# Performance work log

Measured on AMD Instinct MI355X. Metric: run time of the kernel, lower is better.

## Reference

```python
import jax, jax.numpy as jnp
import numpy as np

B, S, R, V, C, K, H = 256, 64, 256, 2000, 10, 6, 4
D = 256
DH = D // H
NEG = -1e9


def setup_inputs() -> dict:
    key = jax.random.key(0)
    ks = jax.random.split(key, 32)
    w = lambda i, shape: jax.random.normal(ks[i], shape, jnp.float32) * 0.05
    inp = {}
    inp["vis_emb"] = jax.random.normal(ks[0], (B * S, D), jnp.float32)
    # multi-hot concept vectors (sparse 0/1)
    inp["basic"] = (jax.random.uniform(ks[1], (R, V)) < 0.01).astype(jnp.float32)
    inp["crucial"] = (jax.random.uniform(ks[2], (R, V)) < 0.01).astype(jnp.float32)
    # to_b / to_k linears
    inp["Wtb"], inp["btb"] = w(3, (V, D)), w(4, (D,))
    inp["Wtk"], inp["btk"] = w(5, (V, D)), w(6, (D,))
    # cross attention (rule2vis): q/k/v/out projections
    inp["Wq"], inp["bq"] = w(7, (D, D)), w(8, (D,))
    inp["Wk"], inp["bk"] = w(9, (D, D)), w(10, (D,))
    inp["Wv"], inp["bv"] = w(11, (D, D)), w(12, (D,))
    inp["Wo"], inp["bo"] = w(13, (D, D)), w(14, (D,))
    # per-class GAT stacks: GAT(256->128), GAT(128->64), Linear(64->K)
    inp["W1"], inp["a1s"], inp["a1d"], inp["b1"] = w(15, (C, D, 128)), w(16, (C, 128)), w(17, (C, 128)), w(18, (C, 128))
    inp["W2"], inp["a2s"], inp["a2d"], inp["b2"] = w(19, (C, 128, 64)), w(20, (C, 64)), w(21, (C, 64)), w(22, (C, 64))
    inp["Wl"], inp["bl"] = w(23, (C, 64, K)), w(24, (C, K))
    # rule-graph adjacency: symmetric + self loops (PyG GATConv adds self loops)
    a0 = jax.random.uniform(ks[25], (R, R)) < 0.05
    inp["adj"] = a0 | a0.T | jnp.eye(R, dtype=bool)
    # class membership mask: each rule node belongs to one class head
    cls = jax.random.randint(ks[26], (R,), 0, C)
    inp["mask"] = (cls[None, :] == jnp.arange(C)[:, None]).astype(jnp.int32)
    return inp


def _gat(h, W, a_s, a_d, b, adj_bias):
    # h: [B,R,Fin] -> [B,R,Fout]; single-head PyG-style GATConv over dense adj
    hW = h @ W                                             # [B,R,F]
    e_dst = jnp.einsum('brf,f->br', hW, a_d)               # dst term
    e_src = jnp.einsum('brf,f->br', hW, a_s)               # src term
    e = jax.nn.leaky_relu(e_dst[:, :, None] + e_src[:, None, :], 0.2)  # [B,Rdst,Rsrc]
    alpha = jax.nn.softmax(e + adj_bias[None], axis=-1)
    return jnp.einsum('bij,bjf->bif', alpha, hW) + b


def reference(vis_emb, basic, crucial, Wtb, btb, Wtk, btk, Wq, bq, Wk, bk, Wv, bv,
              Wo, bo, W1, a1s, a1d, b1, W2, a2s, a2d, b2, Wl, bl, adj, mask):
    # rule embeddings: to_b(basic) + to_k(crucial)
    rule = basic @ Wtb + btb + crucial @ Wtk + btk         # [R,D]
    kv = vis_emb.reshape(B, S, D)
    q = jnp.broadcast_to(rule[None], (B, R, D))
    Q = (q @ Wq + bq).reshape(B, R, H, DH)
    Kx = (kv @ Wk + bk).reshape(B, S, H, DH)
    Vx = (kv @ Wv + bv).reshape(B, S, H, DH)
    att = jnp.einsum('brhd,bshd->bhrs', Q, Kx) / jnp.sqrt(jnp.float32(DH))
    att = jax.nn.softmax(att, axis=-1)
    emb = jnp.einsum('bhrs,bshd->brhd', att, Vx).reshape(B, R, D) @ Wo + bo  # [B,R,D]

    adj_bias = jnp.where(adj, 0.0, NEG).astype(emb.dtype)  # [R,R]
    outs = []
    for c in range(C):  # small fixed number of class heads
        h = emb * mask[c].astype(emb.dtype)[None, :, None]
        h = jax.nn.relu(_gat(h, W1[c], a1s[c], a1d[c], b1[c], adj_bias))
        h = _gat(h, W2[c], a2s[c], a2d[c], b2[c], adj_bias)  # dropout = eval identity
        h = h @ Wl[c] + bl[c]                                # [B,R,K]
        outs.append(jax.nn.log_softmax(h.sum(axis=1), axis=1))
    return jnp.stack(outs)  # [C,B,K]
```

## Files before the change

kernel.cpp:

```cpp
#include <hip/hip_runtime.h>
#include <stdint.h>

#define NB 256
#define NS 64
#define NR 256
#define NV 2000
#define NC 10
#define NK 6
#define ND 256

typedef __attribute__((ext_vector_type(8))) short bf16x8;
typedef __attribute__((ext_vector_type(4))) float f32x4;

__device__ __forceinline__ float bf2f(uint16_t u) {
  return __uint_as_float(((uint32_t)u) << 16);
}
__device__ __forceinline__ uint16_t f2bf(float f) {
  uint32_t x = __float_as_uint(f);
  x += 0x7FFFu + ((x >> 16) & 1u);
  return (uint16_t)(x >> 16);
}

__global__ __launch_bounds__(256) void k_front(
    const void* __restrict__ adj_raw, const int* __restrict__ mask,
    const float* __restrict__ W2, const float* __restrict__ a2s,
    const float* __restrict__ a2d,
    uint32_t* __restrict__ adjbits, int* __restrict__ cls,
    int* __restrict__ lists, int* __restrict__ cnt,
    int* __restrict__ deg, uint8_t* __restrict__ nbr,
    int8_t* __restrict__ midx,
    float* __restrict__ ud2, float* __restrict__ us2,
    const float* __restrict__ Wo, const float* __restrict__ Wk,
    const float* __restrict__ Wv, const float* __restrict__ W1,
    uint16_t* __restrict__ WOT, uint16_t* __restrict__ WKVT,
    uint16_t* __restrict__ W1T,
    const float* __restrict__ basic, const float* __restrict__ cruc,
    const float* __restrict__ Wtb, const float* __restrict__ btb,
    const float* __restrict__ Wtk, const float* __restrict__ btk,
    const float* __restrict__ Wq, const float* __restrict__ bq,
    uint16_t* __restrict__ Qbf,
    const float* __restrict__ vis, const float* __restrict__ bk,
    const float* __restrict__ bv,
    uint16_t* __restrict__ KX, uint16_t* __restrict__ VX)
{
  __shared__ char smem[33792];
  int bid = blockIdx.x;
  int tid = threadIdx.x;
  if (bid < 11) {
    if (bid == 0) {
      int* s_is4 = (int*)smem;
      if (tid == 0) *s_is4 = 1;
      __syncthreads();
      const uint32_t* u = (const uint32_t*)adj_raw;
      int ok = 1;
      for (int idx = tid; idx < 16384; idx += 256) {
        uint32_t v = u[idx];
        if (!(v == 0u || v == 1u || v == 0x3F800000u)) ok = 0;
      }
      if (!ok) atomicAnd(s_is4, 0);
      __syncthreads();
      int is4 = *s_is4;
      const uint8_t* b8 = (const uint8_t*)adj_raw;
      int dg = 0;
      for (int w = 0; w < 8; ++w) {
        uint32_t word = 0;
        for (int jb = 0; jb < 32; ++jb) {
          int j = w * 32 + jb;
          int bit = is4 ? (u[tid * 256 + j] != 0u) : (b8[tid * 256 + j] != 0);
          if (bit) {
            word |= (1u << jb);
            if (dg < 64) nbr[tid * 64 + dg] = (uint8_t)j;
            dg++;
          }
        }
        adjbits[tid * 8 + w] = word;
      }
      deg[tid] = (dg > 64) ? 64 : dg;
      int c = 0;
      for (int cc = 0; cc < NC; ++cc) if (mask[cc * 256 + tid] != 0) c = cc;
      cls[tid] = c;
      __syncthreads();
      if (tid == 0) {
        int cn[NC];
        for (int i = 0; i < NC; ++i) cn[i] = 0;
        for (int r = 0; r < 256; ++r) {
          int cc = cls[r];
          if (cn[cc] < 64) lists[cc * 64 + cn[cc]] = r;
          cn[cc]++;
        }
        for (int i = 0; i < NC; ++i) cnt[i] = (cn[i] > 64) ? 64 : cn[i];
        for (int i = 0; i < NC * 256; ++i) midx[i] = -1;
        for (int cc = 0; cc < NC; ++cc)
          for (int i = 0; i < cnt[cc]; ++i)
            midx[cc * 256 + lists[cc * 64 + i]] = (int8_t)i;
      }
    } else {
      int c = bid - 1;
      if (tid < 128) {
        float s1 = 0.f, s2 = 0.f;
        for (int g = 0; g < 64; ++g) {
          float w = W2[(c * 128 + tid) * 64 + g];
          s1 += w * a2d[c * 64 + g];
          s2 += w * a2s[c * 64 + g];
        }
        ud2[c * 128 + tid] = s1;
        us2[c * 128 + tid] = s2;
      }
    }
  } else if (bid < 139) {
    float (*ts)[65] = (float(*)[65])smem;
    int pb = bid - 11;
    const float* src;
    uint16_t* dst;
    int ncols, kt, nt;
    if (pb < 16)      { src = Wo; dst = WOT; ncols = 256; kt = pb >> 2; nt = pb & 3; }
    else if (pb < 32) { int t = pb - 16; src = Wk; dst = WKVT; ncols = 256; kt = t >> 2; nt = t & 3; }
    else if (pb < 48) { int t = pb - 32; src = Wv; dst = WKVT + 256 * 256; ncols = 256; kt = t >> 2; nt = t & 3; }
    else { int t = pb - 48; int c = t >> 3; int tt = t & 7;
           src = W1 + (long)c * 256 * 128; dst = W1T + (long)c * 128 * 256;
           ncols = 128; kt = tt >> 1; nt = tt & 1; }
    for (int idx = tid; idx < 4096; idx += 256) {
      int i = idx >> 6, j = idx & 63;
      ts[i][j] = src[(long)(kt * 64 + i) * ncols + nt * 64 + j];
    }
    __syncthreads();
    for (int idx = tid; idx < 4096; idx += 256) {
      int i = idx >> 6, j = idx & 63;
      dst[(long)(nt * 64 + i) * 256 + kt * 64 + j] = f2bf(ts[j][i]);
    }
  } else if (bid < 395) {
    float* row_s  = (float*)smem;
    float* rule_s = row_s + 2048;
    int*   nzi    = (int*)(rule_s + 256);
    float* nzv    = (float*)(nzi + 128);
    int*   nzcp   = (int*)(nzv + 128);
    int r = bid - 139;
    float acc = btb[tid] + btk[tid];
    for (int m = 0; m < 2; ++m) {
      const float* src = m ? cruc : basic;
      const float* W   = m ? Wtk : Wtb;
      for (int idx = tid; idx < 2048; idx += 256)
        row_s[idx] = (idx < NV) ? src[r * NV + idx] : 0.0f;
      if (tid == 0) *nzcp = 0;
      __syncthreads();
      if (tid < 64) {
        int base = 0;
        for (int ch = 0; ch < 32; ++ch) {
          int idx = ch * 64 + tid;
          float v = row_s[idx];
          unsigned long long bm = __ballot(v != 0.0f);
          if (v != 0.0f) {
            int pos = base + (int)__popcll(bm & ((1ull << tid) - 1ull));
            if (pos < 128) { nzi[pos] = idx; nzv[pos] = v; }
          }
          base += (int)__popcll(bm);
        }
        if (tid == 0) *nzcp = (base > 128) ? 128 : base;
      }
      __syncthreads();
      int n = *nzcp;
      for (int t = 0; t < n; ++t) acc += nzv[t] * W[nzi[t] * 256 + tid];
      __syncthreads();
    }
    rule_s[tid] = acc;
    __syncthreads();
    float q = bq[tid];
    for (int k2 = 0; k2 < 256; ++k2) q += rule_s[k2] * Wq[k2 * 256 + tid];
    Qbf[r * 256 + tid] = f2bf(q * 0.125f);
  } else {
    uint16_t* A_s = (uint16_t*)smem;
    int t = bid - 395;
    int bx = t & 255, by = t >> 8;
    int lane = tid & 63, w = tid >> 6;
    int r15 = lane & 15, kg = lane >> 4;
    long m0 = (long)bx * 64;
    int n0 = by * 64 + w * 16;
    for (int idx = tid; idx < 2048; idx += 256) {
      int r = idx >> 5, ch = idx & 31;
      const float4* p = (const float4*)&vis[(m0 + r) * 256 + ch * 8];
      float4 v0 = p[0], v1 = p[1];
      uint4 wd;
      wd.x = (uint32_t)f2bf(v0.x) | ((uint32_t)f2bf(v0.y) << 16);
      wd.y = (uint32_t)f2bf(v0.z) | ((uint32_t)f2bf(v0.w) << 16);
      wd.z = (uint32_t)f2bf(v1.x) | ((uint32_t)f2bf(v1.y) << 16);
      wd.w = (uint32_t)f2bf(v1.z) | ((uint32_t)f2bf(v1.w) << 16);
      *(uint4*)&A_s[r * 264 + ch * 8] = wd;
    }
    __syncthreads();
    const uint16_t* bptr = &WKVT[(long)(n0 + r15) * 256 + kg * 8];
    f32x4 acc[4];
    #pragma unroll
    for (int mt = 0; mt < 4; ++mt) acc[mt] = (f32x4){0.f, 0.f, 0.f, 0.f};
    #pragma unroll
    for (int ks = 0; ks < 8; ++ks) {
      bf16x8 bfr = *(const bf16x8*)(bptr + ks * 32);
      #pragma unroll
      for (int mt = 0; mt < 4; ++mt) {
        bf16x8 afr = *(const bf16x8*)&A_s[(mt * 16 + r15) * 264 + kg * 8 + ks * 32];
        acc[mt] = __builtin_amdgcn_mfma_f32_16x16x32_bf16(afr, bfr, acc[mt], 0, 0, 0);
      }
    }
    int col = n0 + r15;
    float bb = (col < 256) ? bk[col] : bv[col - 256];
    uint16_t* outp = (col < 256) ? KX : VX;
    int oc = (col < 256) ? col : col - 256;
    #pragma unroll
    for (int mt = 0; mt < 4; ++mt)
      #pragma unroll
      for (int j = 0; j < 4; ++j) {
        long row = m0 + mt * 16 + kg * 4 + j;
        outp[row * 256 + oc] = f2bf(acc[mt][j] + bb);
      }
  }
}

__global__ __launch_bounds__(512) void k_attn(const uint16_t* __restrict__ Qbf,
                         const uint16_t* __restrict__ KX, const uint16_t* __restrict__ VX,
                         uint16_t* __restrict__ EMB)
{
  __shared__ uint16_t p_s[128 * 72];
  __shared__ uint16_t vt_s[64 * 72];
  int tid = threadIdx.x;
  int lane = tid & 63, w = tid >> 6;
  int r15 = lane & 15, kg = lane >> 4;
  int b = blockIdx.x >> 1;
  int rbase = (blockIdx.x & 1) * 128;
  for (int h = 0; h < 4; ++h) {
    __syncthreads();
    for (int idx = tid; idx < 2048; idx += 512) {
      int s = idx >> 5, d2 = (idx & 31) * 2;
      uint32_t v = *(const uint32_t*)&VX[((long)(b * 64 + s)) * 256 + h * 64 + d2];
      vt_s[d2 * 72 + s] = (uint16_t)(v & 0xffff);
      vt_s[(d2 + 1) * 72 + s] = (uint16_t)(v >> 16);
    }
    __syncthreads();
    f32x4 sacc[4];
    #pragma unroll
    for (int nt = 0; nt < 4; ++nt) sacc[nt] = (f32x4){0.f, 0.f, 0.f, 0.f};
    #pragma unroll
    for (int ks = 0; ks < 2; ++ks) {
      bf16x8 afr = *(const bf16x8*)&Qbf[(long)(rbase + w * 16 + r15) * 256 + h * 64 + ks * 32 + kg * 8];
      #pragma unroll
      for (int nt = 0; nt < 4; ++nt) {
        bf16x8 bfr = *(const bf16x8*)&KX[((long)(b * 64 + nt * 16 + r15)) * 256 + h * 64 + ks * 32 + kg * 8];
        sacc[nt] = __builtin_amdgcn_mfma_f32_16x16x32_bf16(afr, bfr, sacc[nt], 0, 0, 0);
      }
    }
    #pragma unroll
    for (int j = 0; j < 4; ++j) {
      float m = sacc[0][j];
      #pragma unroll
      for (int nt = 1; nt < 4; ++nt) m = fmaxf(m, sacc[nt][j]);
      m = fmaxf(m, __shfl_xor(m, 1));
      m = fmaxf(m, __shfl_xor(m, 2));
      m = fmaxf(m, __shfl_xor(m, 4));
      m = fmaxf(m, __shfl_xor(m, 8));
      float pv[4];
      float sum = 0.f;
      #pragma unroll
      for (int nt = 0; nt < 4; ++nt) { pv[nt] = __expf(sacc[nt][j] - m); sum += pv[nt]; }
      sum += __shfl_xor(sum, 1);
      sum += __shfl_xor(sum, 2);
      sum += __shfl_xor(sum, 4);
      sum += __shfl_xor(sum, 8);
      float rs = 1.0f / sum;
      #pragma unroll
      for (int nt = 0; nt < 4; ++nt)
        p_s[(w * 16 + kg * 4 + j) * 72 + nt * 16 + r15] = f2bf(pv[nt] * rs);
    }
    f32x4 oacc[4];
    #pragma unroll
    for (int nt = 0; nt < 4; ++nt) oacc[nt] = (f32x4){0.f, 0.f, 0.f, 0.f};
    #pragma unroll
    for (int ks = 0; ks < 2; ++ks) {
      bf16x8 afr = *(const bf16x8*)&p_s[(w * 16 + r15) * 72 + ks * 32 + kg * 8];
      #pragma unroll
      for (int nt = 0; nt < 4; ++nt) {
        bf16x8 bfr = *(const bf16x8*)&vt_s[(nt * 16 + r15) * 72 + ks * 32 + kg * 8];
        oacc[nt] = __builtin_amdgcn_mfma_f32_16x16x32_bf16(afr, bfr, oacc[nt], 0, 0, 0);
      }
    }
    #pragma unroll
    for (int nt = 0; nt < 4; ++nt)
      #pragma unroll
      for (int j = 0; j < 4; ++j) {
        long row = (long)(b * 256 + rbase + w * 16 + kg * 4 + j);
        EMB[row * 256 + h * 64 + nt * 16 + r15] = f2bf(oacc[nt][j]);
      }
  }
}

__global__ __launch_bounds__(256) void k_wo(uint16_t* __restrict__ EMB,
                    const uint16_t* __restrict__ WOT, const float* __restrict__ bo)
{
  __shared__ uint16_t A_s[64 * 264];
  int tid = threadIdx.x;
  int lane = tid & 63, w = tid >> 6;
  int r15 = lane & 15, kg = lane >> 4;
  long m0 = (long)blockIdx.x * 64;
  for (int idx = tid; idx < 2048; idx += 256) {
    int r = idx >> 5, ch = idx & 31;
    uint4 v = *(const uint4*)&EMB[(m0 + r) * 256 + ch * 8];
    *(uint4*)&A_s[r * 264 + ch * 8] = v;
  }
  __syncthreads();
  #pragma unroll
  for (int nt = 0; nt < 4; ++nt) {
    int n0 = nt * 64 + w * 16;
    const uint16_t* bptr = &WOT[(long)(n0 + r15) * 256 + kg * 8];
    f32x4 acc[4];
    #pragma unroll
    for (int mt = 0; mt < 4; ++mt) acc[mt] = (f32x4){0.f, 0.f, 0.f, 0.f};
    #pragma unroll
    for (int ks = 0; ks < 8; ++ks) {
      bf16x8 bfr = *(const bf16x8*)(bptr + ks * 32);
      #pragma unroll
      for (int mt = 0; mt < 4; ++mt) {
        bf16x8 afr = *(const bf16x8*)&A_s[(mt * 16 + r15) * 264 + kg * 8 + ks * 32];
        acc[mt] = __builtin_amdgcn_mfma_f32_16x16x32_bf16(afr, bfr, acc[mt], 0, 0, 0);
      }
    }
    int col = n0 + r15;
    float bb = bo[col];
    #pragma unroll
    for (int mt = 0; mt < 4; ++mt)
      #pragma unroll
      for (int j = 0; j < 4; ++j) {
        long row = m0 + mt * 16 + kg * 4 + j;
        EMB[row * 256 + col] = f2bf(acc[mt][j] + bb);
      }
  }
}

__global__ __launch_bounds__(1024) void k_gat(
    const uint16_t* __restrict__ EMB, const uint16_t* __restrict__ W1T,
    const float* __restrict__ a1d, const float* __restrict__ a1s,
    const int* __restrict__ lists, const int* __restrict__ cnt_g,
    const int* __restrict__ deg_g, const uint8_t* __restrict__ nbr_g,
    const int8_t* __restrict__ midx_g,
    const float* __restrict__ b1, const float* __restrict__ ud2_g,
    const float* __restrict__ us2_g, const float* __restrict__ W2,
    const float* __restrict__ b2, const float* __restrict__ Wl,
    const float* __restrict__ bl, float* __restrict__ out)
{
  __shared__ uint16_t alpha_s[256 * 72];
  __shared__ uint16_t hwt_s[128 * 72];
  __shared__ float e1d_s[256], e1s_s[256], rd1_s[256];
  __shared__ float e2d_s[256], e2s_s[256], rd2_s[256];
  __shared__ float a1d_s[128], a1s_s[128], b1_s[128], ud2_s[128], us2_s[128];
  __shared__ float t_s[128];
  __shared__ int   list_s[64];
  float (*tpart)[128] = (float(*)[128])alpha_s;
  float* wj_s = rd1_s;
  float* svec = (float*)hwt_s;
  float* lvec = (float*)(hwt_s + 256);
  int tid = threadIdx.x;
  int lane = tid & 63, w = tid >> 6;
  int r15 = lane & 15, kg = lane >> 4;
  int c = blockIdx.x >> 8, b = blockIdx.x & 255;
  int n = cnt_g[c];
  if (tid < 64) list_s[tid] = (tid < n) ? lists[c * 64 + tid] : 0;
  if (tid < 128) {
    a1d_s[tid] = a1d[c * 128 + tid];
    a1s_s[tid] = a1s[c * 128 + tid];
    b1_s[tid]  = b1[c * 128 + tid];
    ud2_s[tid] = ud2_g[c * 128 + tid];
    us2_s[tid] = us2_g[c * 128 + tid];
  }
  if (tid < 256) { e1d_s[tid] = 0.f; e1s_s[tid] = 0.f; }
  int r = tid >> 2, q = tid & 3;
  int dg = deg_g[r];
  int t0 = q * 16;
  int ncnt = dg - t0; ncnt = (ncnt < 0) ? 0 : (ncnt > 16 ? 16 : ncnt);
  const uint32_t* np = (const uint32_t*)&nbr_g[r * 64 + t0];
  uint32_t nbw0 = np[0], nbw1 = np[1], nbw2 = np[2], nbw3 = np[3];
  __syncthreads();
  int mt = w & 3, nh = w >> 2;
  int colA = nh * 32 + r15, colB = colA + 16;
  const uint16_t* bptr = &W1T[((long)c * 128 + colA) * 256 + kg * 8];
  const uint16_t* arow = &EMB[((long)b * 256 + list_s[mt * 16 + r15]) * 256 + kg * 8];
  f32x4 acc0 = (f32x4){0.f, 0.f, 0.f, 0.f};
  f32x4 acc1 = (f32x4){0.f, 0.f, 0.f, 0.f};
  if (mt * 16 < n) {
    #pragma unroll
    for (int ks = 0; ks < 8; ++ks) {
      bf16x8 b0 = *(const bf16x8*)(bptr + ks * 32);
      bf16x8 b1f = *(const bf16x8*)(bptr + 16 * 256 + ks * 32);
      bf16x8 afr = *(const bf16x8*)(arow + ks * 32);
      acc0 = __builtin_amdgcn_mfma_f32_16x16x32_bf16(afr, b0, acc0, 0, 0, 0);
      acc1 = __builtin_amdgcn_mfma_f32_16x16x32_bf16(afr, b1f, acc1, 0, 0, 0);
    }
  }
  {
    uint2 pA, pB;
    pA.x = (uint32_t)f2bf(acc0[0]) | ((uint32_t)f2bf(acc0[1]) << 16);
    pA.y = (uint32_t)f2bf(acc0[2]) | ((uint32_t)f2bf(acc0[3]) << 16);
    pB.x = (uint32_t)f2bf(acc1[0]) | ((uint32_t)f2bf(acc1[1]) << 16);
    pB.y = (uint32_t)f2bf(acc1[2]) | ((uint32_t)f2bf(acc1[3]) << 16);
    *(uint2*)&hwt_s[colA * 72 + mt * 16 + kg * 4] = pA;
    *(uint2*)&hwt_s[colB * 72 + mt * 16 + kg * 4] = pB;
    float adA = a1d_s[colA], adB = a1d_s[colB];
    float asA = a1s_s[colA], asB = a1s_s[colB];
    #pragma unroll
    for (int j = 0; j < 4; ++j) {
      float pd = acc0[j] * adA + acc1[j] * adB;
      float ps = acc0[j] * asA + acc1[j] * asB;
      pd += __shfl_xor(pd, 1); pd += __shfl_xor(pd, 2);
      pd += __shfl_xor(pd, 4); pd += __shfl_xor(pd, 8);
      ps += __shfl_xor(ps, 1); ps += __shfl_xor(ps, 2);
      ps += __shfl_xor(ps, 4); ps += __shfl_xor(ps, 8);
      if (r15 == 0) {
        int jm = mt * 16 + kg * 4 + j;
        e2d_s[nh * 64 + jm] = pd;
        e2s_s[nh * 64 + jm] = ps;
      }
    }
  }
  __syncthreads();
  for (int idx = tid; idx < 4608; idx += 1024)
    *(uint2*)&alpha_s[idx * 4] = (uint2){0u, 0u};
  if (tid < 64 && tid < n) {
    float sd = e2d_s[tid] + e2d_s[tid + 64] + e2d_s[tid + 128] + e2d_s[tid + 192];
    float ss = e2s_s[tid] + e2s_s[tid + 64] + e2s_s[tid + 128] + e2s_s[tid + 192];
    int rr = list_s[tid];
    e1d_s[rr] = sd;
    e1s_s[rr] = ss;
  }
  __syncthreads();
  {
    float e1dv = e1d_s[r];
    float den = 0.f;
    #define NB_CHUNK(WORD, BASE)                                            \
      _Pragma("unroll")                                                     \
      for (int ii = 0; ii < 4; ++ii) {                                      \
        if (BASE + ii < ncnt) {                                             \
          int j = (int)((WORD >> (ii * 8)) & 255u);                         \
          float e = e1dv + e1s_s[j];                                        \
          e = fmaxf(e, 0.2f * e);                                           \
          e = fminf(e, 60.f);                                               \
          float wv = __expf(e);                                             \
          den += wv;                                                        \
          int mi = midx_g[c * 256 + j];                                     \
          if (mi >= 0) alpha_s[r * 72 + mi] = f2bf(wv);                     \
        }                                                                   \
      }
    NB_CHUNK(nbw0, 0) NB_CHUNK(nbw1, 4) NB_CHUNK(nbw2, 8) NB_CHUNK(nbw3, 12)
    #undef NB_CHUNK
    den += __shfl_xor(den, 1);
    den += __shfl_xor(den, 2);
    if (q == 0) rd1_s[r] = 1.0f / den;
  }
  __syncthreads();
  f32x4 g[8];
  #pragma unroll
  for (int nt = 0; nt < 8; ++nt) g[nt] = (f32x4){0.f, 0.f, 0.f, 0.f};
  int kslices = (n > 32) ? 2 : 1;
  for (int ks = 0; ks < kslices; ++ks) {
    bf16x8 afr = *(const bf16x8*)&alpha_s[(w * 16 + r15) * 72 + ks * 32 + kg * 8];
    #pragma unroll
    for (int nt = 0; nt < 8; ++nt) {
      bf16x8 bfr = *(const bf16x8*)&hwt_s[(nt * 16 + r15) * 72 + ks * 32 + kg * 8];
      g[nt] = __builtin_amdgcn_mfma_f32_16x16x32_bf16(afr, bfr, g[nt], 0, 0, 0);
    }
  }
  {
    float rd1v[4];
    #pragma unroll
    for (int j = 0; j < 4; ++j) rd1v[j] = rd1_s[w * 16 + kg * 4 + j];
    float ed[4] = {0.f, 0.f, 0.f, 0.f}, es[4] = {0.f, 0.f, 0.f, 0.f};
    #pragma unroll
    for (int nt = 0; nt < 8; ++nt) {
      float uf = ud2_s[nt * 16 + r15], sf = us2_s[nt * 16 + r15];
      float bf = b1_s[nt * 16 + r15];
      #pragma unroll
      for (int j = 0; j < 4; ++j) {
        float gv = fmaxf(g[nt][j] * rd1v[j] + bf, 0.f);
        g[nt][j] = gv;
        ed[j] += gv * uf;
        es[j] += gv * sf;
      }
    }
    __syncthreads();
    #pragma unroll
    for (int j = 0; j < 4; ++j) {
      ed[j] += __shfl_xor(ed[j], 1); ed[j] += __shfl_xor(ed[j], 2);
      ed[j] += __shfl_xor(ed[j], 4); ed[j] += __shfl_xor(ed[j], 8);
      es[j] += __shfl_xor(es[j], 1); es[j] += __shfl_xor(es[j], 2);
      es[j] += __shfl_xor(es[j], 4); es[j] += __shfl_xor(es[j], 8);
      if (r15 == 0) {
        e2d_s[w * 16 + kg * 4 + j] = ed[j];
        e2s_s[w * 16 + kg * 4 + j] = es[j];
      }
    }
  }
  __syncthreads();
  {
    float e2dv = e2d_s[r];
    float den2 = 0.f;
    #define NB_CHUNK(WORD, BASE)                                            \
      _Pragma("unroll")                                                     \
      for (int ii = 0; ii < 4; ++ii) {                                      \
        if (BASE + ii < ncnt) {                                             \
          int j = (int)((WORD >> (ii * 8)) & 255u);                         \
          float e = e2dv + e2s_s[j];                                        \
          e = fmaxf(e, 0.2f * e);                                           \
          e = fminf(e, 60.f);                                               \
          den2 += __expf(e);                                                \
        }                                                                   \
      }
    NB_CHUNK(nbw0, 0) NB_CHUNK(nbw1, 4) NB_CHUNK(nbw2, 8) NB_CHUNK(nbw3, 12)
    #undef NB_CHUNK
    den2 += __shfl_xor(den2, 1);
    den2 += __shfl_xor(den2, 2);
    if (q == 0) rd2_s[r] = 1.0f / den2;
  }
  __syncthreads();
  {
    float e2sv = e2s_s[r];
    float wj = 0.f;
    #define NB_CHUNK(WORD, BASE)                                            \
      _Pragma("unroll")                                                     \
      for (int ii = 0; ii < 4; ++ii) {                                      \
        if (BASE + ii < ncnt) {                                             \
          int i2 = (int)((WORD >> (ii * 8)) & 255u);                        \
          float e = e2d_s[i2] + e2sv;                                       \
          e = fmaxf(e, 0.2f * e);                                           \
          e = fminf(e, 60.f);                                               \
          wj += __expf(e) * rd2_s[i2];                                      \
        }                                                                   \
      }
    NB_CHUNK(nbw0, 0) NB_CHUNK(nbw1, 4) NB_CHUNK(nbw2, 8) NB_CHUNK(nbw3, 12)
    #undef NB_CHUNK
    wj += __shfl_xor(wj, 1);
    wj += __shfl_xor(wj, 2);
    if (q == 0) wj_s[r] = wj;
  }
  __syncthreads();
  {
    float wjv[4];
    #pragma unroll
    for (int j = 0; j < 4; ++j) wjv[j] = wj_s[w * 16 + kg * 4 + j];
    #pragma unroll
    for (int nt = 0; nt < 8; ++nt) {
      float tp = wjv[0] * g[nt][0] + wjv[1] * g[nt][1] + wjv[2] * g[nt][2] + wjv[3] * g[nt][3];
      tp += __shfl_xor(tp, 16);
      tp += __shfl_xor(tp, 32);
      if (kg == 0) tpart[w][nt * 16 + r15] = tp;
    }
  }
  __syncthreads();
  if (tid < 128) {
    float s = 0.f;
    #pragma unroll
    for (int w2 = 0; w2 < 16; ++w2) s += tpart[w2][tid];
    t_s[tid] = s;
  }
  __syncthreads();
  {
    int col = tid & 63, fg = tid >> 6;
    float sp = 0.f;
    #pragma unroll
    for (int i = 0; i < 8; ++i) {
      int f = fg * 8 + i;
      sp += t_s[f] * W2[((long)c * 128 + f) * 64 + col];
    }
    tpart[fg][col] = sp;
  }
  __syncthreads();
  if (tid < 64) {
    float s = 256.0f * b2[c * 64 + tid];
    #pragma unroll
    for (int fg = 0; fg < 16; ++fg) s += tpart[fg][tid];
    svec[tid] = s;
  }
  __syncthreads();
  if (tid < 6) {
    float lg = 256.0f * bl[c * 6 + tid];
    for (int f = 0; f < 64; ++f) lg += svec[f] * Wl[((long)c * 64 + f) * 6 + tid];
    lvec[tid] = lg;
  }
  __syncthreads();
  if (tid == 0) {
    float mm = lvec[0];
    for (int k2 = 1; k2 < 6; ++k2) mm = fmaxf(mm, lvec[k2]);
    float ss = 0.f;
    for (int k2 = 0; k2 < 6; ++k2) ss += __expf(lvec[k2] - mm);
    float lse = mm + __logf(ss);
    for (int k2 = 0; k2 < 6; ++k2) out[((long)c * 256 + b) * 6 + k2] = lvec[k2] - lse;
  }
}

extern "C" void kernel_launch(void* const* d_in, const int* in_sizes, int n_in,
                              void* d_out, int out_size, void* d_ws, size_t ws_size,
                              hipStream_t stream)
{
  const float* vis   = (const float*)d_in[0];
  const float* basic = (const float*)d_in[1];
  const float* cruc  = (const float*)d_in[2];
  const float* Wtb   = (const float*)d_in[3];
  const float* btb   = (const float*)d_in[4];
  const float* Wtk   = (const float*)d_in[5];
  const float* btk   = (const float*)d_in[6];
  const float* Wq    = (const float*)d_in[7];
  const float* bq    = (const float*)d_in[8];
  const float* Wk    = (const float*)d_in[9];
  const float* bk    = (const float*)d_in[10];
  const float* Wv    = (const float*)d_in[11];
  const float* bv    = (const float*)d_in[12];
  const float* Wo    = (const float*)d_in[13];
  const float* bo    = (const float*)d_in[14];
  const float* W1    = (const float*)d_in[15];
  const float* a1s   = (const float*)d_in[16];
  const float* a1d   = (const float*)d_in[17];
  const float* b1    = (const float*)d_in[18];
  const float* W2    = (const float*)d_in[19];
  const float* a2s   = (const float*)d_in[20];
  const float* a2d   = (const float*)d_in[21];
  const float* b2    = (const float*)d_in[22];
  const float* Wl    = (const float*)d_in[23];
  const float* bl    = (const float*)d_in[24];
  const void*  adj   = d_in[25];
  const int*   mask  = (const int*)d_in[26];
  float* out = (float*)d_out;
  char* ws = (char*)d_ws;

  uint16_t* QBF  = (uint16_t*)(ws + 0);
  uint32_t* ADJ  = (uint32_t*)(ws + 262144);
  int*      CLS  = (int*)(ws + 270336);
  int*      LST  = (int*)(ws + 271360);
  int*      CNT  = (int*)(ws + 273920);
  int*      DEG  = (int*)(ws + 273984);
  uint8_t*  NBR  = (uint8_t*)(ws + 275008);
  int8_t*   MIDX = (int8_t*)(ws + 291392);
  float*    UD2  = (float*)(ws + 293952);
  float*    US2  = (float*)(ws + 299072);
  uint16_t* WOT  = (uint16_t*)(ws + 304192);
  uint16_t* WKVT = (uint16_t*)(ws + 435264);
  uint16_t* W1T  = (uint16_t*)(ws + 697408);
  uint16_t* KX   = (uint16_t*)(ws + 1352768);
  uint16_t* VX   = (uint16_t*)(ws + 9741376);
  uint16_t* EMB  = (uint16_t*)(ws + 18129984);

  hipLaunchKernelGGL(k_front, dim3(2443), dim3(256), 0, stream,
                     adj, mask, W2, a2s, a2d, ADJ, CLS, LST, CNT, DEG, NBR, MIDX,
                     UD2, US2,
                     Wo, Wk, Wv, W1, WOT, WKVT, W1T,
                     basic, cruc, Wtb, btb, Wtk, btk, Wq, bq, QBF,
                     vis, bk, bv, KX, VX);
  hipLaunchKernelGGL(k_attn, dim3(512), dim3(512), 0, stream, QBF, KX, VX, EMB);
  hipLaunchKernelGGL(k_wo, dim3(1024), dim3(256), 0, stream, EMB, WOT, bo);
  hipLaunchKernelGGL(k_gat, dim3(2560), dim3(1024), 0, stream,
                     EMB, W1T, a1d, a1s, LST, CNT, DEG, NBR, MIDX,
                     b1, UD2, US2, W2, b2, Wl, bl, out);
}
```

Measured before the change: 416.8 us.

## Process two batch elements per GAT block to amortize per-class setup

Each k_gat block now handles a pair of batch elements (A and B) for one class, halving the grid to 1280 blocks. Class constants, W1T fragments and neighbor lists are loaded once and reused for both, interleaving twice the MFMA and exp work between barriers for more ILP. midx is staged in shared memory instead of read from global. This doubles LDS use and register pressure (two sets of g accumulators), which may reduce occupancy to one block per CU.

```diff
diff --git a/kernel.cpp b/kernel.cpp
--- a/kernel.cpp
+++ b/kernel.cpp
@@ -343,23 +343,35 @@
     const float* __restrict__ b2, const float* __restrict__ Wl,
     const float* __restrict__ bl, float* __restrict__ out)
 {
-  __shared__ uint16_t alpha_s[256 * 72];
-  __shared__ uint16_t hwt_s[128 * 72];
-  __shared__ float e1d_s[256], e1s_s[256], rd1_s[256];
-  __shared__ float e2d_s[256], e2s_s[256], rd2_s[256];
+  __shared__ uint16_t alphaA[256 * 72], alphaB[256 * 72];
+  __shared__ uint16_t hwtA[128 * 72], hwtB[128 * 72];
+  __shared__ float e1dA_s[256], e1sA_s[256], e1dB_s[256], e1sB_s[256];
+  __shared__ float rd1A_s[256], rd1B_s[256];
+  __shared__ float e2dA_s[256], e2sA_s[256], e2dB_s[256], e2sB_s[256];
+  __shared__ float rd2A_s[256], rd2B_s[256];
   __shared__ float a1d_s[128], a1s_s[128], b1_s[128], ud2_s[128], us2_s[128];
-  __shared__ float t_s[128];
+  __shared__ float t_sA[128], t_sB[128];
   __shared__ int   list_s[64];
-  float (*tpart)[128] = (float(*)[128])alpha_s;
-  float* wj_s = rd1_s;
-  float* svec = (float*)hwt_s;
-  float* lvec = (float*)(hwt_s + 256);
+  __shared__ int8_t midx_s[256];
+  float (*tpartA)[128] = (float(*)[128])alphaA;
+  float (*tpartB)[128] = (float(*)[128])alphaB;
+  float* wjA_s = rd1A_s;
+  float* wjB_s = rd1B_s;
+  float* svecA = (float*)hwtA;
+  float* lvecA = (float*)(hwtA + 256);
+  float* svecB = (float*)hwtB;
+  float* lvecB = (float*)(hwtB + 256);
   int tid = threadIdx.x;
   int lane = tid & 63, w = tid >> 6;
   int r15 = lane & 15, kg = lane >> 4;
-  int c = blockIdx.x >> 8, b = blockIdx.x & 255;
+  int c = blockIdx.x >> 7, bp = blockIdx.x & 127;
+  int bA = bp * 2, bB = bp * 2 + 1;
   int n = cnt_g[c];
   if (tid < 64) list_s[tid] = (tid < n) ? lists[c * 64 + tid] : 0;
+  if (tid >= 64 && tid < 128) {
+    int i = tid - 64;
+    ((uint32_t*)midx_s)[i] = ((const uint32_t*)(midx_g + (long)c * 256))[i];
+  }
   if (tid < 128) {
     a1d_s[tid] = a1d[c * 128 + tid];
     a1s_s[tid] = a1s[c * 128 + tid];
@@ -367,7 +379,10 @@
     ud2_s[tid] = ud2_g[c * 128 + tid];
     us2_s[tid] = us2_g[c * 128 + tid];
   }
-  if (tid < 256) { e1d_s[tid] = 0.f; e1s_s[tid] = 0.f; }
+  if (tid < 256) {
+    e1dA_s[tid] = 0.f; e1sA_s[tid] = 0.f;
+    e1dB_s[tid] = 0.f; e1sB_s[tid] = 0.f;
+  }
   int r = tid >> 2, q = tid & 3;
   int dg = deg_g[r];
   int t0 = q * 16;
@@ -378,215 +393,297 @@
   int mt = w & 3, nh = w >> 2;
   int colA = nh * 32 + r15, colB = colA + 16;
   const uint16_t* bptr = &W1T[((long)c * 128 + colA) * 256 + kg * 8];
-  const uint16_t* arow = &EMB[((long)b * 256 + list_s[mt * 16 + r15]) * 256 + kg * 8];
-  f32x4 acc0 = (f32x4){0.f, 0.f, 0.f, 0.f};
-  f32x4 acc1 = (f32x4){0.f, 0.f, 0.f, 0.f};
+  const uint16_t* arA = &EMB[((long)bA * 256 + list_s[mt * 16 + r15]) * 256 + kg * 8];
+  const uint16_t* arB = &EMB[((long)bB * 256 + list_s[mt * 16 + r15]) * 256 + kg * 8];
+  f32x4 aA0 = (f32x4){0.f,0.f,0.f,0.f}, aA1 = (f32x4){0.f,0.f,0.f,0.f};
+  f32x4 aB0 = (f32x4){0.f,0.f,0.f,0.f}, aB1 = (f32x4){0.f,0.f,0.f,0.f};
   if (mt * 16 < n) {
     #pragma unroll
     for (int ks = 0; ks < 8; ++ks) {
       bf16x8 b0 = *(const bf16x8*)(bptr + ks * 32);
       bf16x8 b1f = *(const bf16x8*)(bptr + 16 * 256 + ks * 32);
-      bf16x8 afr = *(const bf16x8*)(arow + ks * 32);
-      acc0 = __builtin_amdgcn_mfma_f32_16x16x32_bf16(afr, b0, acc0, 0, 0, 0);
-      acc1 = __builtin_amdgcn_mfma_f32_16x16x32_bf16(afr, b1f, acc1, 0, 0, 0);
+      bf16x8 afA = *(const bf16x8*)(arA + ks * 32);
+      bf16x8 afB = *(const bf16x8*)(arB + ks * 32);
+      aA0 = __builtin_amdgcn_mfma_f32_16x16x32_bf16(afA, b0, aA0, 0, 0, 0);
+      aA1 = __builtin_amdgcn_mfma_f32_16x16x32_bf16(afA, b1f, aA1, 0, 0, 0);
+      aB0 = __builtin_amdgcn_mfma_f32_16x16x32_bf16(afB, b0, aB0, 0, 0, 0);
+      aB1 = __builtin_amdgcn_mfma_f32_16x16x32_bf16(afB, b1f, aB1, 0, 0, 0);
     }
   }
   {
-    uint2 pA, pB;
-    pA.x = (uint32_t)f2bf(acc0[0]) | ((uint32_t)f2bf(acc0[1]) << 16);
-    pA.y = (uint32_t)f2bf(acc0[2]) | ((uint32_t)f2bf(acc0[3]) << 16);
-    pB.x = (uint32_t)f2bf(acc1[0]) | ((uint32_t)f2bf(acc1[1]) << 16);
-    pB.y = (uint32_t)f2bf(acc1[2]) | ((uint32_t)f2bf(acc1[3]) << 16);
-    *(uint2*)&hwt_s[colA * 72 + mt * 16 + kg * 4] = pA;
-    *(uint2*)&hwt_s[colB * 72 + mt * 16 + kg * 4] = pB;
+    uint2 pk;
+    pk.x = (uint32_t)f2bf(aA0[0]) | ((uint32_t)f2bf(aA0[1]) << 16);
+    pk.y = (uint32_t)f2bf(aA0[2]) | ((uint32_t)f2bf(aA0[3]) << 16);
+    *(uint2*)&hwtA[colA * 72 + mt * 16 + kg * 4] = pk;
+    pk.x = (uint32_t)f2bf(aA1[0]) | ((uint32_t)f2bf(aA1[1]) << 16);
+    pk.y = (uint32_t)f2bf(aA1[2]) | ((uint32_t)f2bf(aA1[3]) << 16);
+    *(uint2*)&hwtA[colB * 72 + mt * 16 + kg * 4] = pk;
+    pk.x = (uint32_t)f2bf(aB0[0]) | ((uint32_t)f2bf(aB0[1]) << 16);
+    pk.y = (uint32_t)f2bf(aB0[2]) | ((uint32_t)f2bf(aB0[3]) << 16);
+    *(uint2*)&hwtB[colA * 72 + mt * 16 + kg * 4] = pk;
+    pk.x = (uint32_t)f2bf(aB1[0]) | ((uint32_t)f2bf(aB1[1]) << 16);
+    pk.y = (uint32_t)f2bf(aB1[2]) | ((uint32_t)f2bf(aB1[3]) << 16);
+    *(uint2*)&hwtB[colB * 72 + mt * 16 + kg * 4] = pk;
     float adA = a1d_s[colA], adB = a1d_s[colB];
     float asA = a1s_s[colA], asB = a1s_s[colB];
     #pragma unroll
     for (int j = 0; j < 4; ++j) {
-      float pd = acc0[j] * adA + acc1[j] * adB;
-      float ps = acc0[j] * asA + acc1[j] * asB;
-      pd += __shfl_xor(pd, 1); pd += __shfl_xor(pd, 2);
-      pd += __shfl_xor(pd, 4); pd += __shfl_xor(pd, 8);
-      ps += __shfl_xor(ps, 1); ps += __shfl_xor(ps, 2);
-      ps += __shfl_xor(ps, 4); ps += __shfl_xor(ps, 8);
+      float pdA = aA0[j] * adA + aA1[j] * adB;
+      float psA = aA0[j] * asA + aA1[j] * asB;
+      float pdB = aB0[j] * adA + aB1[j] * adB;
+      float psB = aB0[j] * asA + aB1[j] * asB;
+      pdA += __shfl_xor(pdA, 1); pdA += __shfl_xor(pdA, 2);
+      pdA += __shfl_xor(pdA, 4); pdA += __shfl_xor(pdA, 8);
+      psA += __shfl_xor(psA, 1); psA += __shfl_xor(psA, 2);
+      psA += __shfl_xor(psA, 4); psA += __shfl_xor(psA, 8);
+      pdB += __shfl_xor(pdB, 1); pdB += __shfl_xor(pdB, 2);
+      pdB += __shfl_xor(pdB, 4); pdB += __shfl_xor(pdB, 8);
+      psB += __shfl_xor(psB, 1); psB += __shfl_xor(psB, 2);
+      psB += __shfl_xor(psB, 4); psB += __shfl_xor(psB, 8);
       if (r15 == 0) {
         int jm = mt * 16 + kg * 4 + j;
-        e2d_s[nh * 64 + jm] = pd;
-        e2s_s[nh * 64 + jm] = ps;
-      }
-    }
-  }
-  __syncthreads();
-  for (int idx = tid; idx < 4608; idx += 1024)
-    *(uint2*)&alpha_s[idx * 4] = (uint2){0u, 0u};
+        e2dA_s[nh * 64 + jm] = pdA;
+        e2sA_s[nh * 64 + jm] = psA;
+        e2dB_s[nh * 64 + jm] = pdB;
+        e2sB_s[nh * 64 + jm] = psB;
+      }
+    }
+  }
+  __syncthreads();
+  {
+    uint32_t* zA = (uint32_t*)&alphaA[r * 72 + q * 18];
+    uint32_t* zB = (uint32_t*)&alphaB[r * 72 + q * 18];
+    #pragma unroll
+    for (int i = 0; i < 9; ++i) { zA[i] = 0u; zB[i] = 0u; }
+  }
   if (tid < 64 && tid < n) {
-    float sd = e2d_s[tid] + e2d_s[tid + 64] + e2d_s[tid + 128] + e2d_s[tid + 192];
-    float ss = e2s_s[tid] + e2s_s[tid + 64] + e2s_s[tid + 128] + e2s_s[tid + 192];
+    float sdA = e2dA_s[tid] + e2dA_s[tid + 64] + e2dA_s[tid + 128] + e2dA_s[tid + 192];
+    float ssA = e2sA_s[tid] + e2sA_s[tid + 64] + e2sA_s[tid + 128] + e2sA_s[tid + 192];
+    float sdB = e2dB_s[tid] + e2dB_s[tid + 64] + e2dB_s[tid + 128] + e2dB_s[tid + 192];
+    float ssB = e2sB_s[tid] + e2sB_s[tid + 64] + e2sB_s[tid + 128] + e2sB_s[tid + 192];
     int rr = list_s[tid];
-    e1d_s[rr] = sd;
-    e1s_s[rr] = ss;
+    e1dA_s[rr] = sdA; e1sA_s[rr] = ssA;
+    e1dB_s[rr] = sdB; e1sB_s[rr] = ssB;
   }
   __syncthreads();
   {
-    float e1dv = e1d_s[r];
-    float den = 0.f;
+    float e1dAv = e1dA_s[r], e1dBv = e1dB_s[r];
+    float denA = 0.f, denB = 0.f;
     #define NB_CHUNK(WORD, BASE)                                            \
       _Pragma("unroll")                                                     \
       for (int ii = 0; ii < 4; ++ii) {                                      \
         if (BASE + ii < ncnt) {                                             \
           int j = (int)((WORD >> (ii * 8)) & 255u);                         \
-          float e = e1dv + e1s_s[j];                                        \
-          e = fmaxf(e, 0.2f * e);                                           \
-          e = fminf(e, 60.f);                                               \
-          float wv = __expf(e);                                             \
-          den += wv;                                                        \
-          int mi = midx_g[c * 256 + j];                                     \
-          if (mi >= 0) alpha_s[r * 72 + mi] = f2bf(wv);                     \
+          float eA = e1dAv + e1sA_s[j];                                     \
+          eA = fmaxf(eA, 0.2f * eA); eA = fminf(eA, 60.f);                  \
+          float wA = __expf(eA); denA += wA;                                \
+          float eB = e1dBv + e1sB_s[j];                                     \
+          eB = fmaxf(eB, 0.2f * eB); eB = fminf(eB, 60.f);                  \
+          float wB = __expf(eB); denB += wB;                                \
+          int mi = midx_s[j];                                               \
+          if (mi >= 0) {                                                    \
+            alphaA[r * 72 + mi] = f2bf(wA);                                 \
+            alphaB[r * 72 + mi] = f2bf(wB);                                 \
+          }                                                                 \
         }                                                                   \
       }
     NB_CHUNK(nbw0, 0) NB_CHUNK(nbw1, 4) NB_CHUNK(nbw2, 8) NB_CHUNK(nbw3, 12)
     #undef NB_CHUNK
-    den += __shfl_xor(den, 1);
-    den += __shfl_xor(den, 2);
-    if (q == 0) rd1_s[r] = 1.0f / den;
-  }
-  __syncthreads();
-  f32x4 g[8];
+    denA += __shfl_xor(denA, 1); denA += __shfl_xor(denA, 2);
+    denB += __shfl_xor(denB, 1); denB += __shfl_xor(denB, 2);
+    if (q == 0) { rd1A_s[r] = 1.0f / denA; rd1B_s[r] = 1.0f / denB; }
+  }
+  __syncthreads();
+  f32x4 gA[8], gB[8];
   #pragma unroll
-  for (int nt = 0; nt < 8; ++nt) g[nt] = (f32x4){0.f, 0.f, 0.f, 0.f};
+  for (int nt = 0; nt < 8; ++nt) {
+    gA[nt] = (f32x4){0.f, 0.f, 0.f, 0.f};
+    gB[nt] = (f32x4){0.f, 0.f, 0.f, 0.f};
+  }
   int kslices = (n > 32) ? 2 : 1;
   for (int ks = 0; ks < kslices; ++ks) {
-    bf16x8 afr = *(const bf16x8*)&alpha_s[(w * 16 + r15) * 72 + ks * 32 + kg * 8];
+    bf16x8 afA = *(const bf16x8*)&alphaA[(w * 16 + r15) * 72 + ks * 32 + kg * 8];
+    bf16x8 afB = *(const bf16x8*)&alphaB[(w * 16 + r15) * 72 + ks * 32 + kg * 8];
     #pragma unroll
     for (int nt = 0; nt < 8; ++nt) {
-      bf16x8 bfr = *(const bf16x8*)&hwt_s[(nt * 16 + r15) * 72 + ks * 32 + kg * 8];
-      g[nt] = __builtin_amdgcn_mfma_f32_16x16x32_bf16(afr, bfr, g[nt], 0, 0, 0);
+      bf16x8 bfA = *(const bf16x8*)&hwtA[(nt * 16 + r15) * 72 + ks * 32 + kg * 8];
+      bf16x8 bfB = *(const bf16x8*)&hwtB[(nt * 16 + r15) * 72 + ks * 32 + kg * 8];
+      gA[nt] = __builtin_amdgcn_mfma_f32_16x16x32_bf16(afA, bfA, gA[nt], 0, 0, 0);
+      gB[nt] = __builtin_amdgcn_mfma_f32_16x16x32_bf16(afB, bfB, gB[nt], 0, 0, 0);
     }
   }
   {
-    float rd1v[4];
-    #pragma unroll
-    for (int j = 0; j < 4; ++j) rd1v[j] = rd1_s[w * 16 + kg * 4 + j];
-    float ed[4] = {0.f, 0.f, 0.f, 0.f}, es[4] = {0.f, 0.f, 0.f, 0.f};
+    float rdA[4], rdB[4];
+    #pragma unroll
+    for (int j = 0; j < 4; ++j) {
+      rdA[j] = rd1A_s[w * 16 + kg * 4 + j];
+      rdB[j] = rd1B_s[w * 16 + kg * 4 + j];
+    }
+    float edA[4] = {0.f,0.f,0.f,0.f}, esA[4] = {0.f,0.f,0.f,0.f};
+    float edB[4] = {0.f,0.f,0.f,0.f}, esB[4] = {0.f,0.f,0.f,0.f};
     #pragma unroll
     for (int nt = 0; nt < 8; ++nt) {
       float uf = ud2_s[nt * 16 + r15], sf = us2_s[nt * 16 + r15];
       float bf = b1_s[nt * 16 + r15];
       #pragma unroll
       for (int j = 0; j < 4; ++j) {
-        float gv = fmaxf(g[nt][j] * rd1v[j] + bf, 0.f);
-        g[nt][j] = gv;
-        ed[j] += gv * uf;
-        es[j] += gv * sf;
-      }
-    }
-    __syncthreads();
+        float gvA = fmaxf(gA[nt][j] * rdA[j] + bf, 0.f);
+        gA[nt][j] = gvA;
+        edA[j] += gvA * uf; esA[j] += gvA * sf;
+        float gvB = fmaxf(gB[nt][j] * rdB[j] + bf, 0.f);
+        gB[nt][j] = gvB;
+        edB[j] += gvB * uf; esB[j] += gvB * sf;
+      }
+    }
     #pragma unroll
     for (int j = 0; j < 4; ++j) {
-      ed[j] += __shfl_xor(ed[j], 1); ed[j] += __shfl_xor(ed[j], 2);
-      ed[j] += __shfl_xor(ed[j], 4); ed[j] += __shfl_xor(ed[j], 8);
-      es[j] += __shfl_xor(es[j], 1); es[j] += __shfl_xor(es[j], 2);
-      es[j] += __shfl_xor(es[j], 4); es[j] += __shfl_xor(es[j], 8);
+      edA[j] += __shfl_xor(edA[j], 1); edA[j] += __shfl_xor(edA[j], 2);
+      edA[j] += __shfl_xor(edA[j], 4); edA[j] += __shfl_xor(edA[j], 8);
+      esA[j] += __shfl_xor(esA[j], 1); esA[j] += __shfl_xor(esA[j], 2);
+      esA[j] += __shfl_xor(esA[j], 4); esA[j] += __shfl_xor(esA[j], 8);
+      edB[j] += __shfl_xor(edB[j], 1); edB[j] += __shfl_xor(edB[j], 2);
+      edB[j] += __shfl_xor(edB[j], 4); edB[j] += __shfl_xor(edB[j], 8);
+      esB[j] += __shfl_xor(esB[j], 1); esB[j] += __shfl_xor(esB[j], 2);
+      esB[j] += __shfl_xor(esB[j], 4); esB[j] += __shfl_xor(esB[j], 8);
       if (r15 == 0) {
-        e2d_s[w * 16 + kg * 4 + j] = ed[j];
-        e2s_s[w * 16 + kg * 4 + j] = es[j];
+        int rr = w * 16 + kg * 4 + j;
+        e2dA_s[rr] = edA[j]; e2sA_s[rr] = esA[j];
+        e2dB_s[rr] = edB[j]; e2sB_s[rr] = esB[j];
       }
     }
   }
   __syncthreads();
   {
-    float e2dv = e2d_s[r];
-    float den2 = 0.f;
+    float e2dAv = e2dA_s[r], e2dBv = e2dB_s[r];
+    float dnA = 0.f, dnB = 0.f;
     #define NB_CHUNK(WORD, BASE)                                            \
       _Pragma("unroll")                                                     \
       for (int ii = 0; ii < 4; ++ii) {                                      \
         if (BASE + ii < ncnt) {                                             \
           int j = (int)((WORD >> (ii * 8)) & 255u);                         \
-          float e = e2dv + e2s_s[j];                                        \
-          e = fmaxf(e, 0.2f * e);                                           \
-          e = fminf(e, 60.f);                                               \
-          den2 += __expf(e);                                                \
+          float eA = e2dAv + e2sA_s[j];                                     \
+          eA = fmaxf(eA, 0.2f * eA); eA = fminf(eA, 60.f);                  \
+          dnA += __expf(eA);                                                \
+          float eB = e2dBv + e2sB_s[j];                                     \
+          eB = fmaxf(eB, 0.2f * eB); eB = fminf(eB, 60.f);                  \
+          dnB += __expf(eB);                                                \
         }                                                                   \
       }
     NB_CHUNK(nbw0, 0) NB_CHUNK(nbw1, 4) NB_CHUNK(nbw2, 8) NB_CHUNK(nbw3, 12)
     #undef NB_CHUNK
-    den2 += __shfl_xor(den2, 1);
-    den2 += __shfl_xor(den2, 2);
-    if (q == 0) rd2_s[r] = 1.0f / den2;
+    dnA += __shfl_xor(dnA, 1); dnA += __shfl_xor(dnA, 2);
+    dnB += __shfl_xor(dnB, 1); dnB += __shfl_xor(dnB, 2);
+    if (q == 0) { rd2A_s[r] = 1.0f / dnA; rd2B_s[r] = 1.0f / dnB; }
   }
   __syncthreads();
   {
-    float e2sv = e2s_s[r];
-    float wj = 0.f;
+    float e2sAv = e2sA_s[r], e2sBv = e2sB_s[r];
+    float wjA = 0.f, wjB = 0.f;
     #define NB_CHUNK(WORD, BASE)                                            \
       _Pragma("unroll")                                                     \
       for (int ii = 0; ii < 4; ++ii) {                                      \
         if (BASE + ii < ncnt) {                                             \
           int i2 = (int)((WORD >> (ii * 8)) & 255u);                        \
-          float e = e2d_s[i2] + e2sv;                                       \
-          e = fmaxf(e, 0.2f * e);                                           \
-          e = fminf(e, 60.f);                                               \
-          wj += __expf(e) * rd2_s[i2];                                      \
+          float eA = e2dA_s[i2] + e2sAv;                                    \
+          eA = fmaxf(eA, 0.2f * eA); eA = fminf(eA, 60.f);                  \
+          wjA += __expf(eA) * rd2A_s[i2];                                   \
+          float eB = e2dB_s[i2] + e2sBv;                                    \
+          eB = fmaxf(eB, 0.2f * eB); eB = fminf(eB, 60.f);                  \
+          wjB += __expf(eB) * rd2B_s[i2];                                   \
         }                                                                   \
       }
     NB_CHUNK(nbw0, 0) NB_CHUNK(nbw1, 4) NB_CHUNK(nbw2, 8) NB_CHUNK(nbw3, 12)
     #undef NB_CHUNK
-    wj += __shfl_xor(wj, 1);
-    wj += __shfl_xor(wj, 2);
-    if (q == 0) wj_s[r] = wj;
+    wjA += __shfl_xor(wjA, 1); wjA += __shfl_xor(wjA, 2);
+    wjB += __shfl_xor(wjB, 1); wjB += __shfl_xor(wjB, 2);
+    if (q == 0) { wjA_s[r] = wjA; wjB_s[r] = wjB; }
   }
   __syncthreads();
   {
-    float wjv[4];
-    #pragma unroll
-    for (int j = 0; j < 4; ++j) wjv[j] = wj_s[w * 16 + kg * 4 + j];
+    float wvA[4], wvB[4];
+    #pragma unroll
+    for (int j = 0; j < 4; ++j) {
+      wvA[j] = wjA_s[w * 16 + kg * 4 + j];
+      wvB[j] = wjB_s[w * 16 + kg * 4 + j];
+    }
     #pragma unroll
     for (int nt = 0; nt < 8; ++nt) {
-      float tp = wjv[0] * g[nt][0] + wjv[1] * g[nt][1] + wjv[2] * g[nt][2] + wjv[3] * g[nt][3];
-      tp += __shfl_xor(tp, 16);
-      tp += __shfl_xor(tp, 32);
-      if (kg == 0) tpart[w][nt * 16 + r15] = tp;
+      float tpA = wvA[0]*gA[nt][0] + wvA[1]*gA[nt][1] + wvA[2]*gA[nt][2] + wvA[3]*gA[nt][3];
+      float tpB = wvB[0]*gB[nt][0] + wvB[1]*gB[nt][1] + wvB[2]*gB[nt][2] + wvB[3]*gB[nt][3];
+      tpA += __shfl_xor(tpA, 16); tpA += __shfl_xor(tpA, 32);
+      tpB += __shfl_xor(tpB, 16); tpB += __shfl_xor(tpB, 32);
+      if (kg == 0) {
+        tpartA[w][nt * 16 + r15] = tpA;
+        tpartB[w][nt * 16 + r15] = tpB;
+      }
     }
   }
   __syncthreads();
   if (tid < 128) {
     float s = 0.f;
     #pragma unroll
-    for (int w2 = 0; w2 < 16; ++w2) s += tpart[w2][tid];
-    t_s[tid] = s;
+    for (int w2 = 0; w2 < 16; ++w2) s += tpartA[w2][tid];
+    t_sA[tid] = s;
+  } else if (tid < 256) {
+    int f = tid - 128;
+    float s = 0.f;
+    #pragma unroll
+    for (int w2 = 0; w2 < 16; ++w2) s += tpartB[w2][f];
+    t_sB[f] = s;
   }
   __syncthreads();
   {
-    int col = tid & 63, fg = tid >> 6;
+    int batch = tid >> 9;
+    int tt = tid & 511;
+    int col = tt & 63, fg = tt >> 6;
+    const float* tsrc = batch ? t_sB : t_sA;
     float sp = 0.f;
     #pragma unroll
-    for (int i = 0; i < 8; ++i) {
-      int f = fg * 8 + i;
-      sp += t_s[f] * W2[((long)c * 128 + f) * 64 + col];
-    }
-    tpart[fg][col] = sp;
+    for (int i = 0; i < 16; ++i) {
+      int f = fg * 16 + i;
+      sp += tsrc[f] * W2[((long)c * 128 + f) * 64 + col];
+    }
+    if (batch) tpartB[fg][col] = sp; else tpartA[fg][col] = sp;
   }
   __syncthreads();
   if (tid < 64) {
     float s = 256.0f * b2[c * 64 + tid];
     #pragma unroll
-    for (int fg = 0; fg < 16; ++fg) s += tpart[fg][tid];
-    svec[tid] = s;
+    for (int fg = 0; fg < 8; ++fg) s += tpartA[fg][tid];
+    svecA[tid] = s;
+  } else if (tid >= 512 && tid < 576) {
+    int col = tid - 512;
+    float s = 256.0f * b2[c * 64 + col];
+    #pragma unroll
+    for (int fg = 0; fg < 8; ++fg) s += tpartB[fg][col];
+    svecB[col] = s;
   }
   __syncthreads();
   if (tid < 6) {
     float lg = 256.0f * bl[c * 6 + tid];
-    for (int f = 0; f < 64; ++f) lg += svec[f] * Wl[((long)c * 64 + f) * 6 + tid];
-    lvec[tid] = lg;
+    for (int f = 0; f < 64; ++f) lg += svecA[f] * Wl[((long)c * 64 + f) * 6 + tid];
+    lvecA[tid] = lg;
+  } else if (tid >= 512 && tid < 518) {
+    int k = tid - 512;
+    float lg = 256.0f * bl[c * 6 + k];
+    for (int f = 0; f < 64; ++f) lg += svecB[f] * Wl[((long)c * 64 + f) * 6 + k];
+    lvecB[k] = lg;
   }
   __syncthreads();
   if (tid == 0) {
-    float mm = lvec[0];
-    for (int k2 = 1; k2 < 6; ++k2) mm = fmaxf(mm, lvec[k2]);
+    float mm = lvecA[0];
+    for (int k2 = 1; k2 < 6; ++k2) mm = fmaxf(mm, lvecA[k2]);
     float ss = 0.f;
-    for (int k2 = 0; k2 < 6; ++k2) ss += __expf(lvec[k2] - mm);
+    for (int k2 = 0; k2 < 6; ++k2) ss += __expf(lvecA[k2] - mm);
     float lse = mm + __logf(ss);
-    for (int k2 = 0; k2 < 6; ++k2) out[((long)c * 256 + b) * 6 + k2] = lvec[k2] - lse;
+    for (int k2 = 0; k2 < 6; ++k2) out[((long)c * 256 + bA) * 6 + k2] = lvecA[k2] - lse;
+  } else if (tid == 512) {
+    float mm = lvecB[0];
+    for (int k2 = 1; k2 < 6; ++k2) mm = fmaxf(mm, lvecB[k2]);
+    float ss = 0.f;
+    for (int k2 = 0; k2 < 6; ++k2) ss += __expf(lvecB[k2] - mm);
+    float lse = mm + __logf(ss);
+    for (int k2 = 0; k2 < 6; ++k2) out[((long)c * 256 + bB) * 6 + k2] = lvecB[k2] - lse;
   }
 }
 
@@ -649,7 +746,7 @@
                      vis, bk, bv, KX, VX);
   hipLaunchKernelGGL(k_attn, dim3(512), dim3(512), 0, stream, QBF, KX, VX, EMB);
   hipLaunchKernelGGL(k_wo, dim3(1024), dim3(256), 0, stream, EMB, WOT, bo);
-  hipLaunchKernelGGL(k_gat, dim3(2560), dim3(1024), 0, stream,
+  hipLaunchKernelGGL(k_gat, dim3(1280), dim3(1024), 0, stream,
                      EMB, W1T, a1d, a1s, LST, CNT, DEG, NBR, MIDX,
                      b1, UD2, US2, W2, b2, Wl, bl, out);
 }
```

Result: faster. 361.0 us (-13.4%).
